# Kernel optimization log

Measured on AMD Instinct MI355X. Metric: run time of the kernel, lower is better.

Reference implementation:

```python
import math
import jax
import jax.numpy as jnp
from jax import lax
import numpy as np

B, T, S, C, E = 16, 1024, 2048, 256, 256
STRIDE, MAX_SAMPLES, SIGMA, RAND_START = 20, 20, 3.0, 0


def setup_inputs():
    key = jax.random.key(0)
    ks = jax.random.split(key, 6)
    return {
        "x": jax.random.normal(ks[0], (B, T, C), jnp.float32),
        "target_embedding": jax.random.normal(ks[1], (B, T, E), jnp.float32),
        # scale keys so pre-softmax scores are O(1..10) like a trained model
        "enc_keys": jax.random.normal(ks[2], (B, E, S), jnp.float32) * 0.05,
        "enc_values": jax.random.normal(ks[3], (B, S, E), jnp.float32),
        "W_in": jax.random.normal(ks[4], (E, C), jnp.float32) * math.sqrt(1.0 / C),
        "b_in": jnp.zeros((E,), jnp.float32),
        "W_out": jax.random.normal(ks[5], (C, E), jnp.float32) * math.sqrt(1.0 / E),
        "b_out": jnp.zeros((C,), jnp.float32),
    }


def _get_matrix(attn, sim_vec, stride, start):
    # attn: [B,T,S], sim_vec: [B,S,E]
    nrm = sim_vec / jnp.linalg.norm(sim_vec, axis=2, keepdims=True)
    attn_avg = jnp.mean(attn, axis=1)[..., None]          # [B,S,1]
    ns = nrm[:, start::stride, :]                          # [B,N,E]
    aa = attn_avg[:, start::stride, :]                     # [B,N,1]
    sim = jnp.einsum('bne,bme->bnm', ns, ns)               # cosine similarity
    qual = aa @ jnp.swapaxes(aa, 1, 2)                     # quality outer product
    return qual * sim                                      # DPP kernel L [B,N,N]


def _bfgm(L, max_samples):
    # Vectorized faithful version of the greedy Cholesky DPP MAP loop.
    Bv, N, _ = L.shape
    bidx = jnp.arange(Bv)
    D0 = jnp.diagonal(L, axis1=1, axis2=2)                 # [B,N]
    mask0 = jnp.ones((Bv, N), L.dtype)
    J0 = jnp.argmax(jnp.log(D0 * mask0), axis=1)
    mask0 = mask0.at[bidx, J0].set(0.0)
    C0 = jnp.zeros((Bv, N, max_samples), L.dtype)          # col 0 stays zero (as in torch)

    def step(carry, t):
        Cm, D, J, mask = carry
        Lj = L[bidx, J, :]                                 # [B,N] = L[b, J[b], i]
        cj = Cm[bidx, J, :]                                # [B,K]
        cdot = jnp.einsum('bnk,bk->bn', Cm, cj)            # <c_i, c_j>
        dj = D[bidx, J][:, None]
        e = (Lj - cdot) / dj * mask                        # zero at already-selected
        Cm = Cm.at[:, :, t].set(e)
        D = D - e * e
        J = jnp.argmax(jnp.log(D * mask), axis=1)
        mask = mask.at[bidx, J].set(0.0)
        return (Cm, D, J, mask), J

    (_, _, _, _), Js = lax.scan(step, (C0, D0, J0, mask0), jnp.arange(1, max_samples))
    all_J = jnp.concatenate([J0[None, :], Js], axis=0).T   # [B,max_samples]
    return jnp.sort(all_J, axis=1)                         # = nonzero(1-mask) order


def _create_gm(mu, sigma, length):
    pos = jnp.arange(length, dtype=jnp.float32)            # [S]
    z = pos[None, None, :] - mu[:, :, None].astype(jnp.float32)
    g = jnp.exp(-(z * z) / (2.0 * sigma * sigma)) / (math.sqrt(2.0 * math.pi) * sigma)
    return jnp.sum(g, axis=1)                              # [B,S]


def _forward(x, target_embedding, enc_keys, enc_values, W_in, b_in, W_out, b_out):
    residual = x
    h = (jnp.einsum('btc,ec->bte', x, W_in) + b_in + target_embedding) * math.sqrt(0.5)
    scores = jnp.einsum('bte,bes->bts', h, enc_keys)       # [B,T,S]
    attn = jax.nn.softmax(scores, axis=-1)
    # DPP auxiliary KL loss (training path, encoder_padding_mask=None); the
    # kernel / greedy selection / target distribution carry no gradient.
    L = _get_matrix(lax.stop_gradient(attn), lax.stop_gradient(enc_values), STRIDE, RAND_START)
    mu = _bfgm(L, MAX_SAMPLES)
    dist = jax.nn.softmax(_create_gm(mu, SIGMA, scores.shape[2]), axis=1)
    x_mean = jnp.mean(attn, axis=1)                        # [B,S]
    kl = jnp.sum(x_mean * (jnp.log(x_mean) - dist))        # KLDivLoss(input=dist, target=x_mean, sum)
    out = jnp.einsum('bts,bse->bte', attn, enc_values)
    s = enc_values.shape[1]
    out = out * (s * math.sqrt(1.0 / s))                   # = sqrt(s)
    out = (jnp.einsum('bte,ce->btc', out, W_out) + b_out + residual) * math.sqrt(0.5)
    return out, attn, -kl


def reference(x, target_embedding, enc_keys, enc_values, W_in, b_in, W_out, b_out):
    return _forward(x, target_embedding, enc_keys, enc_values, W_in, b_in, W_out, b_out)
```

## Files before the change

### kernel.cpp

```cpp
#include <hip/hip_runtime.h>
#include <math.h>

#define BB 16
#define TT 1024
#define SS 2048
#define CC 256
#define EE 256
#define NSUB 103
#define MAXS 20
#define STRIDE_ 20
#define XCH 32

static constexpr float RSQRT2  = 0.70710678118654752440f;
static constexpr float SQRT_S  = 45.25483399593904f;
static constexpr float GNORM   = 0.13298076013381093f;
static constexpr float INV2S2  = 0.055555555555555555f;

typedef __attribute__((ext_vector_type(8))) __bf16 bf16x8;
typedef __attribute__((ext_vector_type(4))) float  f32x4;

__device__ __forceinline__ float wave_sum(float v) {
    #pragma unroll
    for (int o = 32; o; o >>= 1) v += __shfl_down(v, o);
    return v;
}
__device__ __forceinline__ float wave_max(float v) {
    #pragma unroll
    for (int o = 32; o; o >>= 1) v = fmaxf(v, __shfl_down(v, o));
    return v;
}
__device__ __forceinline__ unsigned short f2bf(float f) {
    unsigned int u = __float_as_uint(f);
    u = (u + 0x7FFFu + ((u >> 16) & 1u)) >> 16;
    return (unsigned short)u;
}
__device__ __forceinline__ float bf2f(unsigned short s) {
    return __uint_as_float(((unsigned int)s) << 16);
}

#define GLD_LDS16(g, l) __builtin_amdgcn_global_load_lds(                      \
    (const __attribute__((address_space(1))) void*)(g),                        \
    (__attribute__((address_space(3))) void*)(l), 16, 0, 0)

__global__ __launch_bounds__(256) void k_cast3(
    const float* __restrict__ a,  unsigned short* __restrict__ oa, int na,
    const float* __restrict__ b2, unsigned short* __restrict__ ob, int nb,
    const float* __restrict__ c2, unsigned short* __restrict__ oc, int nc)
{
    int i = blockIdx.x * 256 + threadIdx.x;
    const float* in; unsigned short* out;
    if (i < na)                { in = a;  out = oa; }
    else if (i < na + nb)      { in = b2; out = ob; i -= na; }
    else if (i < na + nb + nc) { in = c2; out = oc; i -= na + nb; }
    else return;
    const float4 v = reinterpret_cast<const float4*>(in)[i];
    union { unsigned short u[4]; unsigned long long v8; } pk;
    pk.u[0] = f2bf(v.x); pk.u[1] = f2bf(v.y);
    pk.u[2] = f2bf(v.z); pk.u[3] = f2bf(v.w);
    reinterpret_cast<unsigned long long*>(out)[i] = pk.v8;
}

__global__ __launch_bounds__(256) void k_transpose_bf16(
    const float* __restrict__ in, unsigned short* __restrict__ out, int R, int Cc)
{
    __shared__ float t[64][65];
    const int b = blockIdx.z;
    const int r0 = blockIdx.x * 64, c0 = blockIdx.y * 64;
    const float* ip = in + (size_t)b * R * Cc;
    unsigned short* op = out + (size_t)b * R * Cc;
    const int tx = threadIdx.x & 63, ty = threadIdx.x >> 6;
    #pragma unroll
    for (int i = 0; i < 16; ++i)
        t[ty + 4 * i][tx] = ip[(size_t)(r0 + ty + 4 * i) * Cc + c0 + tx];
    __syncthreads();
    #pragma unroll
    for (int i = 0; i < 16; ++i)
        op[(size_t)(c0 + ty + 4 * i) * R + r0 + tx] = f2bf(t[tx][ty + 4 * i]);
}

template<int BM, int BN, int MODE>
__global__ __launch_bounds__(256) void k_gemm(
    const unsigned short* __restrict__ Abase,
    const unsigned short* __restrict__ Btbase,
    const float* __restrict__ bias, const float* __restrict__ add,
    float* __restrict__ Obase, unsigned short* __restrict__ Obbase,
    int M, int Nn, int K, float scale)
{
    constexpr int BK = 64;
    constexpr int AR = BM / 32;
    constexpr int BR = BN / 32;
    constexpr int WM = BM / 2, WN = BN / 2;
    constexpr int MI = WM / 16, NJ = WN / 16;

    __shared__ unsigned short As[BM * BK];
    __shared__ unsigned short Bs[BN * BK];

    const int nwg = gridDim.x * gridDim.y * gridDim.z;
    int l = blockIdx.x + gridDim.x * (blockIdx.y + gridDim.y * blockIdx.z);
    if ((nwg & 7) == 0) l = (l & 7) * (nwg >> 3) + (l >> 3);
    const int bx = l % gridDim.x; l /= gridDim.x;
    const int by = l % gridDim.y;
    const int b  = l / gridDim.y;

    const int m0 = bx * BM;
    const int n0 = by * BN;
    const unsigned short* A  = Abase  + (size_t)b * M  * K;
    const unsigned short* Bt = Btbase + (size_t)b * Nn * K;

    const int tid  = threadIdx.x;
    const int w    = tid >> 6;
    const int lane = tid & 63;
    const int wm   = w & 1, wn = w >> 1;

    const int sr  = tid >> 3;
    const int skb = ((tid & 7) << 4) ^ ((sr & 7) << 4);
    const unsigned short* ga[AR];
    const unsigned short* gb[BR];
    #pragma unroll
    for (int p = 0; p < AR; ++p)
        ga[p] = A + (size_t)(m0 + p * 32 + sr) * K + (skb >> 1);
    #pragma unroll
    for (int p = 0; p < BR; ++p)
        gb[p] = Bt + (size_t)(n0 + p * 32 + sr) * K + (skb >> 1);

    const int fr = lane & 15;
    const int qb = (lane >> 4) << 4;

    f32x4 acc[MI][NJ];
    #pragma unroll
    for (int i = 0; i < MI; ++i)
        #pragma unroll
        for (int j = 0; j < NJ; ++j)
            acc[i][j] = (f32x4){0.f, 0.f, 0.f, 0.f};

    for (int k0 = 0; k0 < K; k0 += BK) {
        #pragma unroll
        for (int p = 0; p < AR; ++p) GLD_LDS16(ga[p], As + p * 2048 + w * 512);
        #pragma unroll
        for (int p = 0; p < BR; ++p) GLD_LDS16(gb[p], Bs + p * 2048 + w * 512);
        #pragma unroll
        for (int p = 0; p < AR; ++p) ga[p] += BK;
        #pragma unroll
        for (int p = 0; p < BR; ++p) gb[p] += BK;
        __syncthreads();
        #pragma unroll
        for (int c = 0; c < 2; ++c) {
            bf16x8 af[MI], bf[NJ];
            #pragma unroll
            for (int i = 0; i < MI; ++i) {
                const int row = wm * WM + i * 16 + fr;
                const int byt = row * 128 + ((c * 64 + qb) ^ ((row & 7) << 4));
                af[i] = *reinterpret_cast<const bf16x8*>(
                            reinterpret_cast<const char*>(As) + byt);
            }
            #pragma unroll
            for (int j = 0; j < NJ; ++j) {
                const int row = wn * WN + j * 16 + fr;
                const int byt = row * 128 + ((c * 64 + qb) ^ ((row & 7) << 4));
                bf[j] = *reinterpret_cast<const bf16x8*>(
                            reinterpret_cast<const char*>(Bs) + byt);
            }
            #pragma unroll
            for (int i = 0; i < MI; ++i)
                #pragma unroll
                for (int j = 0; j < NJ; ++j)
                    acc[i][j] = __builtin_amdgcn_mfma_f32_16x16x32_bf16(af[i], bf[j], acc[i][j], 0, 0, 0);
        }
        __syncthreads();
    }

    float* Of = (MODE == 0 || MODE == 1) ? Obase + (size_t)b * M * Nn : nullptr;
    unsigned short* Ob = (MODE == 2 || MODE == 3) ? Obbase + (size_t)b * M * Nn : nullptr;
    const int rb = (lane >> 4) * 4;
    #pragma unroll
    for (int i = 0; i < MI; ++i)
        #pragma unroll
        for (int j = 0; j < NJ; ++j) {
            const int n = n0 + wn * WN + j * 16 + fr;
            #pragma unroll
            for (int r2 = 0; r2 < 4; ++r2) {
                const int m = m0 + wm * WM + i * 16 + rb + r2;
                const size_t idx = (size_t)m * Nn + n;
                if (MODE == 0) {
                    Of[idx] = acc[i][j][r2] * scale;
                } else if (MODE == 1) {
                    Of[idx] = (acc[i][j][r2] + bias[n] + add[idx]) * RSQRT2;
                } else if (MODE == 2) {
                    Ob[idx] = f2bf((acc[i][j][r2] + bias[n] + add[idx]) * RSQRT2);
                } else {
                    Ob[idx] = f2bf(acc[i][j][r2] * scale);
                }
            }
        }
}

__global__ __launch_bounds__(256) void k_softmax(float* __restrict__ attn,
                                                 unsigned short* __restrict__ attnb)
{
    float* p = attn + (size_t)blockIdx.x * SS;
    unsigned short* pb = attnb + (size_t)blockIdx.x * SS;
    const int tid = threadIdx.x;
    __shared__ float w[4];
    union { unsigned short u[8]; uint4 v4; } in;
    in.v4 = *reinterpret_cast<const uint4*>(&pb[tid * 8]);
    float v[8];
    #pragma unroll
    for (int i = 0; i < 8; ++i) v[i] = bf2f(in.u[i]);
    float mx = -INFINITY;
    #pragma unroll
    for (int i = 0; i < 8; ++i) mx = fmaxf(mx, v[i]);
    float wm = wave_max(mx);
    if ((tid & 63) == 0) w[tid >> 6] = wm;
    __syncthreads();
    const float m = fmaxf(fmaxf(w[0], w[1]), fmaxf(w[2], w[3]));
    float s = 0.f;
    #pragma unroll
    for (int i = 0; i < 8; ++i) { v[i] = expf(v[i] - m); s += v[i]; }
    __syncthreads();
    float wsv = wave_sum(s);
    if ((tid & 63) == 0) w[tid >> 6] = wsv;
    __syncthreads();
    const float inv = 1.0f / (w[0] + w[1] + w[2] + w[3]);
    float4 o0, o1;
    o0.x = v[0] * inv; o0.y = v[1] * inv; o0.z = v[2] * inv; o0.w = v[3] * inv;
    o1.x = v[4] * inv; o1.y = v[5] * inv; o1.z = v[6] * inv; o1.w = v[7] * inv;
    *reinterpret_cast<float4*>(&p[tid * 8])     = o0;
    *reinterpret_cast<float4*>(&p[tid * 8 + 4]) = o1;
    union { unsigned short u[8]; uint4 v4; } pk;
    pk.u[0] = f2bf(o0.x); pk.u[1] = f2bf(o0.y); pk.u[2] = f2bf(o0.z); pk.u[3] = f2bf(o0.w);
    pk.u[4] = f2bf(o1.x); pk.u[5] = f2bf(o1.y); pk.u[6] = f2bf(o1.z); pk.u[7] = f2bf(o1.w);
    *reinterpret_cast<uint4*>(&pb[tid * 8]) = pk.v4;
}

__global__ __launch_bounds__(256) void k_xmean_part(const unsigned short* __restrict__ attnb,
                                                    float* __restrict__ part)
{
    const int c = blockIdx.x, b = blockIdx.y;
    const unsigned short* p = attnb + ((size_t)b * TT + (size_t)c * (TT / XCH)) * SS
                              + threadIdx.x * 8;
    float acc[8] = {0.f, 0.f, 0.f, 0.f, 0.f, 0.f, 0.f, 0.f};
    #pragma unroll 8
    for (int t = 0; t < TT / XCH; ++t) {
        union { unsigned short u[8]; uint4 v4; } ld;
        ld.v4 = *reinterpret_cast<const uint4*>(p + (size_t)t * SS);
        #pragma unroll
        for (int i = 0; i < 8; ++i) acc[i] += bf2f(ld.u[i]);
    }
    float* o = part + ((size_t)b * XCH + c) * SS + threadIdx.x * 8;
    #pragma unroll
    for (int i = 0; i < 8; ++i) o[i] = acc[i];
}

__global__ __launch_bounds__(256) void k_ns(const float* __restrict__ ev,
                                            const float* __restrict__ part,
                                            float* __restrict__ ns, float* __restrict__ aa,
                                            float* __restrict__ klp)
{
    const int n = blockIdx.x, b = blockIdx.y;
    const int tid = threadIdx.x;
    if (n == 0 && b == 0 && tid == 0) klp[0] = 0.0f;
    const float* rowp = ev + ((size_t)b * SS + (size_t)n * STRIDE_) * EE;
    const float v = rowp[tid];
    __shared__ float w[4];
    float r = wave_sum(v * v);
    if ((tid & 63) == 0) w[tid >> 6] = r;
    float pv = (tid < XCH) ? part[((size_t)b * XCH + tid) * SS + n * STRIDE_] : 0.f;
    float psum = wave_sum(pv);
    __syncthreads();
    const float nrm = sqrtf(w[0] + w[1] + w[2] + w[3]);
    ns[((size_t)b * NSUB + n) * EE + tid] = v / nrm;
    if (tid == 0) aa[b * NSUB + n] = psum * (1.0f / TT);
}

__global__ __launch_bounds__(128) void k_L(const float* __restrict__ ns,
                                           const float* __restrict__ aa,
                                           float* __restrict__ Lm)
{
    const int i = blockIdx.x, b = blockIdx.y;
    const int tid = threadIdx.x;
    __shared__ float nsi[EE];
    nsi[tid]       = ns[((size_t)b * NSUB + i) * EE + tid];
    nsi[tid + 128] = ns[((size_t)b * NSUB + i) * EE + tid + 128];
    __syncthreads();
    const float ai = aa[b * NSUB + i];
    for (int j = tid; j < NSUB; j += 128) {
        const float* rj = ns + ((size_t)b * NSUB + j) * EE;
        float d = 0.f;
        #pragma unroll 4
        for (int e = 0; e < EE; ++e) d += nsi[e] * rj[e];
        Lm[((size_t)b * NSUB + i) * NSUB + j] = d * ai * aa[b * NSUB + j];
    }
}

__global__ __launch_bounds__(256) void k_bfgm_kl(const float* __restrict__ Lm,
                                                 const float* __restrict__ part,
                                                 float* __restrict__ outkl)
{
    const int b = blockIdx.x;
    const int tid = threadIdx.x;
    const float* L = Lm + (size_t)b * NSUB * NSUB;
    __shared__ float D[128], mask[128], Cm[128 * MAXS], cj[MAXS], musS[MAXS];
    __shared__ float rv[4];
    __shared__ int   ri[4];
    __shared__ int   Jsh;
    __shared__ float w[4];
    const bool half = tid < 128;
    const bool act  = tid < NSUB;
    if (half) {
        D[tid]    = act ? L[(size_t)tid * NSUB + tid] : 0.0f;
        mask[tid] = act ? 1.0f : 0.0f;
        #pragma unroll
        for (int k = 0; k < MAXS; ++k) Cm[tid * MAXS + k] = 0.0f;
    }
    __syncthreads();

    auto argmax_step = [&](int t) {
        float key = act ? logf(D[tid] * mask[tid]) : -INFINITY;
        if (isnan(key)) key = INFINITY;
        float v = key; int idx = tid;
        #pragma unroll
        for (int o = 32; o; o >>= 1) {
            float ov = __shfl_down(v, o); int oi = __shfl_down(idx, o);
            if (ov > v || (ov == v && oi < idx)) { v = ov; idx = oi; }
        }
        if ((tid & 63) == 0) { rv[tid >> 6] = v; ri[tid >> 6] = idx; }
        __syncthreads();
        if (tid == 0) {
            float bv = rv[0]; int bi = ri[0];
            #pragma unroll
            for (int q2 = 1; q2 < 4; ++q2)
                if (rv[q2] > bv || (rv[q2] == bv && ri[q2] < bi)) { bv = rv[q2]; bi = ri[q2]; }
            Jsh = bi; mask[bi] = 0.0f; musS[t] = (float)bi;
        }
        __syncthreads();
    };

    argmax_step(0);
    for (int t = 1; t < MAXS; ++t) {
        if (tid < MAXS) cj[tid] = Cm[Jsh * MAXS + tid];
        __syncthreads();
        const int J = Jsh;
        const float dj = D[J];
        float e = 0.0f;
        if (act) {
            const float Ljn = L[(size_t)J * NSUB + tid];
            float cd = 0.f;
            #pragma unroll
            for (int k = 0; k < MAXS; ++k) cd += Cm[tid * MAXS + k] * cj[k];
            e = (Ljn - cd) / dj * mask[tid];
        }
        if (half) { Cm[tid * MAXS + t] = e; D[tid] -= e * e; }
        __syncthreads();
        argmax_step(t);
    }

    float xm[8];
    #pragma unroll
    for (int i = 0; i < 8; ++i) {
        float s = 0.f;
        #pragma unroll 8
        for (int c2 = 0; c2 < XCH; ++c2)
            s += part[((size_t)b * XCH + c2) * SS + tid + (i << 8)];
        xm[i] = s * (1.0f / TT);
    }
    float g[8];
    float mx = -INFINITY;
    #pragma unroll
    for (int i = 0; i < 8; ++i) {
        const float s = (float)(tid + (i << 8));
        float acc = 0.f;
        #pragma unroll
        for (int m = 0; m < MAXS; ++m) { const float z = s - musS[m]; acc += expf(-(z * z) * INV2S2); }
        g[i] = acc * GNORM;
        mx = fmaxf(mx, g[i]);
    }
    float wm = wave_max(mx);
    if ((tid & 63) == 0) w[tid >> 6] = wm;
    __syncthreads();
    const float m = fmaxf(fmaxf(w[0], w[1]), fmaxf(w[2], w[3]));
    float sum = 0.f;
    #pragma unroll
    for (int i = 0; i < 8; ++i) { g[i] = expf(g[i] - m); sum += g[i]; }
    __syncthreads();
    float wsv = wave_sum(sum);
    if ((tid & 63) == 0) w[tid >> 6] = wsv;
    __syncthreads();
    const float inv = 1.0f / (w[0] + w[1] + w[2] + w[3]);
    float acc2 = 0.f;
    #pragma unroll
    for (int i = 0; i < 8; ++i)
        acc2 += xm[i] * (logf(xm[i]) - g[i] * inv);
    __syncthreads();
    float wp = wave_sum(acc2);
    if ((tid & 63) == 0) w[tid >> 6] = wp;
    __syncthreads();
    if (tid == 0) atomicAdd(outkl, -(w[0] + w[1] + w[2] + w[3]));
}

extern "C" void kernel_launch(void* const* d_in, const int* in_sizes, int n_in,
                              void* d_out, int out_size, void* d_ws, size_t ws_size,
                              hipStream_t stream)
{
    const float* x     = (const float*)d_in[0];
    const float* te    = (const float*)d_in[1];
    const float* keys  = (const float*)d_in[2];
    const float* vals  = (const float*)d_in[3];
    const float* W_in  = (const float*)d_in[4];
    const float* b_in  = (const float*)d_in[5];
    const float* W_out = (const float*)d_in[6];
    const float* b_out = (const float*)d_in[7];

    float* outp = (float*)d_out;
    float* attn = outp + (size_t)BB * TT * CC;
    float* klp  = attn + (size_t)BB * TT * SS;

    unsigned short* X       = (unsigned short*)d_ws;
    unsigned short* x_bf    = X;
    unsigned short* Win_bf  = x_bf   + (size_t)BB * TT * CC;
    unsigned short* Wout_bf = Win_bf + (size_t)EE * CC;
    unsigned short* h_bf    = Wout_bf+ (size_t)CC * EE;
    unsigned short* keysT   = h_bf   + (size_t)BB * TT * EE;
    unsigned short* valsT   = keysT  + (size_t)BB * SS * EE;
    unsigned short* attnb   = valsT  + (size_t)BB * EE * SS;
    unsigned short* mid_bf  = attnb  + (size_t)BB * TT * SS;
    float* fws   = (float*)(mid_bf + (size_t)BB * TT * EE + 8);
    float* part  = fws;
    float* ns    = part  + (size_t)BB * XCH * SS;
    float* aa    = ns    + (size_t)BB * NSUB * EE;
    float* Lm    = aa    + (size_t)BB * NSUB;

    {
        const int na = BB * TT * CC / 4, nb = EE * CC / 4, nc = CC * EE / 4;
        const int blocks = (na + nb + nc + 255) / 256;
        k_cast3<<<blocks, 256, 0, stream>>>(x, x_bf, na, W_in, Win_bf, nb, W_out, Wout_bf, nc);
    }
    k_gemm<64, 64, 2><<<dim3(256, 4, 1), 256, 0, stream>>>(
        x_bf, Win_bf, b_in, te, nullptr, h_bf, BB * TT, CC, CC, 1.0f);
    k_transpose_bf16<<<dim3(4, 32, BB), 256, 0, stream>>>(keys, keysT, EE, SS);
    k_gemm<128, 128, 3><<<dim3(8, 16, BB), 256, 0, stream>>>(
        h_bf, keysT, nullptr, nullptr, nullptr, attnb, TT, SS, EE, 1.0f);
    k_transpose_bf16<<<dim3(32, 4, BB), 256, 0, stream>>>(vals, valsT, SS, EE);
    k_softmax<<<BB * TT, 256, 0, stream>>>(attn, attnb);
    k_xmean_part<<<dim3(XCH, BB), 256, 0, stream>>>(attnb, part);
    k_ns<<<dim3(NSUB, BB), 256, 0, stream>>>(vals, part, ns, aa, klp);
    k_L<<<dim3(NSUB, BB), 128, 0, stream>>>(ns, aa, Lm);
    k_bfgm_kl<<<BB, 256, 0, stream>>>(Lm, part, klp);
    k_gemm<64, 128, 3><<<dim3(16, 2, BB), 256, 0, stream>>>(
        attnb, valsT, nullptr, nullptr, nullptr, mid_bf, TT, EE, SS, SQRT_S);
    k_gemm<64, 64, 1><<<dim3(256, 4, 1), 256, 0, stream>>>(
        mid_bf, Wout_bf, b_out, x, outp, nullptr, BB * TT, CC, CC, 1.0f);
}
```

Measured before the change: 460.4 us.

## Merge transposes, use wave-per-row softmax, pad BFGM shared matrix

The separate keys and values transpose launches become one combined launch that picks its tensor from the block index. The softmax now gives each row to a single wavefront holding 32 values per lane, so the block-level shared-memory reductions and barriers are gone and each block covers four rows. The Cm shared array in the greedy DPP kernel is padded to a stride of 21 to reduce LDS bank conflicts. The softmax change raises register pressure per thread.

```diff
diff --git a/kernel.cpp b/kernel.cpp
--- a/kernel.cpp
+++ b/kernel.cpp
@@ -60,12 +60,23 @@
     reinterpret_cast<unsigned long long*>(out)[i] = pk.v8;
 }
 
-__global__ __launch_bounds__(256) void k_transpose_bf16(
-    const float* __restrict__ in, unsigned short* __restrict__ out, int R, int Cc)
+__global__ __launch_bounds__(256) void k_transpose2(
+    const float* __restrict__ keys, unsigned short* __restrict__ keysT,
+    const float* __restrict__ vals, unsigned short* __restrict__ valsT)
 {
     __shared__ float t[64][65];
-    const int b = blockIdx.z;
-    const int r0 = blockIdx.x * 64, c0 = blockIdx.y * 64;
+    const int id = blockIdx.x;
+    const float* in; unsigned short* out;
+    int R, Cc, bx, by, b;
+    if (id < 2048) {
+        in = keys; out = keysT; R = EE; Cc = SS;
+        bx = id & 3; by = (id >> 2) & 31; b = id >> 7;
+    } else {
+        const int id2 = id - 2048;
+        in = vals; out = valsT; R = SS; Cc = EE;
+        bx = id2 & 31; by = (id2 >> 5) & 3; b = id2 >> 7;
+    }
+    const int r0 = bx * 64, c0 = by * 64;
     const float* ip = in + (size_t)b * R * Cc;
     unsigned short* op = out + (size_t)b * R * Cc;
     const int tx = threadIdx.x & 63, ty = threadIdx.x >> 6;
@@ -197,39 +208,44 @@
 __global__ __launch_bounds__(256) void k_softmax(float* __restrict__ attn,
                                                  unsigned short* __restrict__ attnb)
 {
-    float* p = attn + (size_t)blockIdx.x * SS;
-    unsigned short* pb = attnb + (size_t)blockIdx.x * SS;
-    const int tid = threadIdx.x;
-    __shared__ float w[4];
-    union { unsigned short u[8]; uint4 v4; } in;
-    in.v4 = *reinterpret_cast<const uint4*>(&pb[tid * 8]);
-    float v[8];
-    #pragma unroll
-    for (int i = 0; i < 8; ++i) v[i] = bf2f(in.u[i]);
-    float mx = -INFINITY;
-    #pragma unroll
-    for (int i = 0; i < 8; ++i) mx = fmaxf(mx, v[i]);
-    float wm = wave_max(mx);
-    if ((tid & 63) == 0) w[tid >> 6] = wm;
-    __syncthreads();
-    const float m = fmaxf(fmaxf(w[0], w[1]), fmaxf(w[2], w[3]));
+    const int row  = blockIdx.x * 4 + (threadIdx.x >> 6);
+    const int lane = threadIdx.x & 63;
+    float* p = attn + (size_t)row * SS;
+    unsigned short* pb = attnb + (size_t)row * SS;
+
+    float v[32];
+    #pragma unroll
+    for (int s = 0; s < 4; ++s) {
+        union { unsigned short u[8]; uint4 q; } ld;
+        ld.q = *reinterpret_cast<const uint4*>(&pb[s * 512 + lane * 8]);
+        #pragma unroll
+        for (int i = 0; i < 8; ++i) v[s * 8 + i] = bf2f(ld.u[i]);
+    }
+    float mx = v[0];
+    #pragma unroll
+    for (int i = 1; i < 32; ++i) mx = fmaxf(mx, v[i]);
+    #pragma unroll
+    for (int o = 32; o; o >>= 1) mx = fmaxf(mx, __shfl_xor(mx, o));
     float s = 0.f;
     #pragma unroll
-    for (int i = 0; i < 8; ++i) { v[i] = expf(v[i] - m); s += v[i]; }
-    __syncthreads();
-    float wsv = wave_sum(s);
-    if ((tid & 63) == 0) w[tid >> 6] = wsv;
-    __syncthreads();
-    const float inv = 1.0f / (w[0] + w[1] + w[2] + w[3]);
-    float4 o0, o1;
-    o0.x = v[0] * inv; o0.y = v[1] * inv; o0.z = v[2] * inv; o0.w = v[3] * inv;
-    o1.x = v[4] * inv; o1.y = v[5] * inv; o1.z = v[6] * inv; o1.w = v[7] * inv;
-    *reinterpret_cast<float4*>(&p[tid * 8])     = o0;
-    *reinterpret_cast<float4*>(&p[tid * 8 + 4]) = o1;
-    union { unsigned short u[8]; uint4 v4; } pk;
-    pk.u[0] = f2bf(o0.x); pk.u[1] = f2bf(o0.y); pk.u[2] = f2bf(o0.z); pk.u[3] = f2bf(o0.w);
-    pk.u[4] = f2bf(o1.x); pk.u[5] = f2bf(o1.y); pk.u[6] = f2bf(o1.z); pk.u[7] = f2bf(o1.w);
-    *reinterpret_cast<uint4*>(&pb[tid * 8]) = pk.v4;
+    for (int i = 0; i < 32; ++i) { v[i] = expf(v[i] - mx); s += v[i]; }
+    #pragma unroll
+    for (int o = 32; o; o >>= 1) s += __shfl_xor(s, o);
+    const float inv = 1.0f / s;
+    #pragma unroll
+    for (int seg = 0; seg < 4; ++seg) {
+        float4 o0, o1;
+        o0.x = v[seg * 8 + 0] * inv; o0.y = v[seg * 8 + 1] * inv;
+        o0.z = v[seg * 8 + 2] * inv; o0.w = v[seg * 8 + 3] * inv;
+        o1.x = v[seg * 8 + 4] * inv; o1.y = v[seg * 8 + 5] * inv;
+        o1.z = v[seg * 8 + 6] * inv; o1.w = v[seg * 8 + 7] * inv;
+        *reinterpret_cast<float4*>(&p[seg * 512 + lane * 8])     = o0;
+        *reinterpret_cast<float4*>(&p[seg * 512 + lane * 8 + 4]) = o1;
+        union { unsigned short u[8]; uint4 q; } pk;
+        pk.u[0] = f2bf(o0.x); pk.u[1] = f2bf(o0.y); pk.u[2] = f2bf(o0.z); pk.u[3] = f2bf(o0.w);
+        pk.u[4] = f2bf(o1.x); pk.u[5] = f2bf(o1.y); pk.u[6] = f2bf(o1.z); pk.u[7] = f2bf(o1.w);
+        *reinterpret_cast<uint4*>(&pb[seg * 512 + lane * 8]) = pk.q;
+    }
 }
 
 __global__ __launch_bounds__(256) void k_xmean_part(const unsigned short* __restrict__ attnb,
@@ -299,7 +315,7 @@
     const int b = blockIdx.x;
     const int tid = threadIdx.x;
     const float* L = Lm + (size_t)b * NSUB * NSUB;
-    __shared__ float D[128], mask[128], Cm[128 * MAXS], cj[MAXS], musS[MAXS];
+    __shared__ float D[128], mask[128], Cm[128 * 21], cj[MAXS], musS[MAXS];
     __shared__ float rv[4];
     __shared__ int   ri[4];
     __shared__ int   Jsh;
@@ -310,7 +326,7 @@
         D[tid]    = act ? L[(size_t)tid * NSUB + tid] : 0.0f;
         mask[tid] = act ? 1.0f : 0.0f;
         #pragma unroll
-        for (int k = 0; k < MAXS; ++k) Cm[tid * MAXS + k] = 0.0f;
+        for (int k = 0; k < MAXS; ++k) Cm[tid * 21 + k] = 0.0f;
     }
     __syncthreads();
 
@@ -337,7 +353,7 @@
 
     argmax_step(0);
     for (int t = 1; t < MAXS; ++t) {
-        if (tid < MAXS) cj[tid] = Cm[Jsh * MAXS + tid];
+        if (tid < MAXS) cj[tid] = Cm[Jsh * 21 + tid];
         __syncthreads();
         const int J = Jsh;
         const float dj = D[J];
@@ -346,10 +362,10 @@
             const float Ljn = L[(size_t)J * NSUB + tid];
             float cd = 0.f;
             #pragma unroll
-            for (int k = 0; k < MAXS; ++k) cd += Cm[tid * MAXS + k] * cj[k];
+            for (int k = 0; k < MAXS; ++k) cd += Cm[tid * 21 + k] * cj[k];
             e = (Ljn - cd) / dj * mask[tid];
         }
-        if (half) { Cm[tid * MAXS + t] = e; D[tid] -= e * e; }
+        if (half) { Cm[tid * 21 + t] = e; D[tid] -= e * e; }
         __syncthreads();
         argmax_step(t);
     }
@@ -436,11 +452,10 @@
     }
     k_gemm<64, 64, 2><<<dim3(256, 4, 1), 256, 0, stream>>>(
         x_bf, Win_bf, b_in, te, nullptr, h_bf, BB * TT, CC, CC, 1.0f);
-    k_transpose_bf16<<<dim3(4, 32, BB), 256, 0, stream>>>(keys, keysT, EE, SS);
+    k_transpose2<<<4096, 256, 0, stream>>>(keys, keysT, vals, valsT);
     k_gemm<128, 128, 3><<<dim3(8, 16, BB), 256, 0, stream>>>(
         h_bf, keysT, nullptr, nullptr, nullptr, attnb, TT, SS, EE, 1.0f);
-    k_transpose_bf16<<<dim3(32, 4, BB), 256, 0, stream>>>(vals, valsT, SS, EE);
-    k_softmax<<<BB * TT, 256, 0, stream>>>(attn, attnb);
+    k_softmax<<<BB * TT / 4, 256, 0, stream>>>(attn, attnb);
     k_xmean_part<<<dim3(XCH, BB), 256, 0, stream>>>(attnb, part);
     k_ns<<<dim3(NSUB, BB), 256, 0, stream>>>(vals, part, ns, aa, klp);
     k_L<<<dim3(NSUB, BB), 128, 0, stream>>>(ns, aa, Lm);
```

Result: no change. 460.1 us (-0.1%).
